# Kernel optimization log

Measured on AMD Instinct MI355X. Metric: run time of the kernel, lower is better.

Reference implementation:

```python
import jax, jax.numpy as jnp
import numpy as np

N_HEAD = 4
D_K = 64
D_V = 64
D_MODEL = 256
LN_EPS = 1e-5


def setup_inputs() -> dict:
    key = jax.random.key(0)
    k1, k2, k3 = jax.random.split(key, 3)
    B, C, H, W = 2, D_MODEL, 64, 64
    q = jax.random.normal(k1, (B, C, H, W), dtype=jnp.float32)
    # w_qkvs: Linear(d_model, n_head*d_k, bias=False), weight [out, in]
    std_qkv = np.sqrt(2.0 / (D_MODEL + D_K))
    w_qkv = jax.random.normal(k2, (N_HEAD * D_K, D_MODEL), dtype=jnp.float32) * std_qkv
    # fc: Linear(n_head*d_v, d_model), xavier-normal-ish init
    std_fc = np.sqrt(2.0 / (N_HEAD * D_V + D_MODEL))
    fc_w = jax.random.normal(k3, (D_MODEL, N_HEAD * D_V), dtype=jnp.float32) * std_fc
    fc_b = jnp.zeros((D_MODEL,), dtype=jnp.float32)
    ln_g = jnp.ones((D_MODEL,), dtype=jnp.float32)
    ln_b = jnp.zeros((D_MODEL,), dtype=jnp.float32)
    return {"q": q, "w_qkv": w_qkv, "fc_w": fc_w, "fc_b": fc_b, "ln_g": ln_g, "ln_b": ln_b}


def reference(q, w_qkv, fc_w, fc_b, ln_g, ln_b):
    B, C, H, W = q.shape
    L = H * W
    # [B, C, H, W] -> [B, L, C]
    x = q.reshape(B, C, L).transpose(0, 2, 1)
    residual = x
    # shared QKV projection (self-attention branch: q == k == v)
    qkv = x @ w_qkv.T                                  # [B, L, nh*dk]
    qh = qkv.reshape(B, L, N_HEAD, D_K).transpose(2, 0, 1, 3)  # [h, B, L, dk]
    scale = jnp.asarray(np.sqrt(D_K), dtype=q.dtype)
    attn = jnp.einsum('hbqd,hbkd->hbqk', qh, qh) / scale       # [h, B, L, L]
    attn = jax.nn.softmax(attn, axis=-1)
    out = jnp.einsum('hbqk,hbkd->hbqd', attn, qh)              # [h, B, L, dv]
    # [h, B, L, dv] -> [B, L, h*dv]
    out = out.transpose(1, 2, 0, 3).reshape(B, L, N_HEAD * D_V)
    out = out @ fc_w.T + fc_b
    out = out + residual
    mu = jnp.mean(out, axis=-1, keepdims=True)
    var = jnp.mean(jnp.square(out - mu), axis=-1, keepdims=True)
    out = (out - mu) / jnp.sqrt(var + LN_EPS) * ln_g + ln_b
    # raw row-major view back to [B, C, H, W] (matches torch .view)
    return out.reshape(B, -1, H, W)
```

## Files before the change

kernel.cpp:

```cpp
#include <hip/hip_runtime.h>

#define L_SEQ 4096
#define DMODEL 256
#define DH 64
#define NKB 16

typedef __attribute__((ext_vector_type(8))) __bf16 bf16x8;
typedef __attribute__((ext_vector_type(4))) float f32x4;
typedef __attribute__((ext_vector_type(16))) float f32x16;
typedef __attribute__((ext_vector_type(8))) unsigned short ushort8v;
typedef __attribute__((ext_vector_type(4))) unsigned short ushort4v;
typedef __attribute__((ext_vector_type(2))) unsigned int uint2v;
typedef __attribute__((ext_vector_type(4))) unsigned int uint4v;

__device__ __forceinline__ unsigned short f2bf(float f) {
  unsigned u = __builtin_bit_cast(unsigned, f);
  u += 0x7fffu + ((u >> 16) & 1u);
  return (unsigned short)(u >> 16);
}
__device__ __forceinline__ float bf2f(unsigned short h) {
  unsigned u = ((unsigned)h) << 16;
  return __builtin_bit_cast(float, u);
}
__device__ __forceinline__ bf16x8 ld_frag(const unsigned short* p) {
  return __builtin_bit_cast(bf16x8, *(const ushort8v*)p);
}
__device__ __forceinline__ unsigned cvtpk(float lo, float hi) {
  unsigned r;
  asm("v_cvt_pk_bf16_f32 %0, %1, %2" : "=v"(r) : "v"(lo), "v"(hi));
  return r;
}
__device__ __forceinline__ void plswap(unsigned& a, unsigned& b) {
  asm("v_permlane32_swap_b32 %0, %1" : "+v"(a), "+v"(b));
}
__device__ __forceinline__ float exp2raw(float x) {
  float r;
  asm("v_exp_f32 %0, %1" : "=v"(r) : "v"(x));
  return r;
}

__global__ __launch_bounds__(256) void k_transpose(const float* __restrict__ q,
                                                   unsigned short* __restrict__ xbf,
                                                   const float* __restrict__ w,
                                                   const float* __restrict__ fcw,
                                                   unsigned short* __restrict__ wbf,
                                                   unsigned short* __restrict__ fcwbf) {
  int bx = blockIdx.x;
  int t = threadIdx.x;
  if (bx >= 512) {
    int i = ((bx - 512) * 256 + t) * 4;
    float4 a = *(const float4*)(w + i);
    float4 b = *(const float4*)(fcw + i);
    ushort4v av = {f2bf(a.x), f2bf(a.y), f2bf(a.z), f2bf(a.w)};
    ushort4v bv = {f2bf(b.x), f2bf(b.y), f2bf(b.z), f2bf(b.w)};
    *(ushort4v*)(wbf + i) = av;
    *(ushort4v*)(fcwbf + i) = bv;
    return;
  }
  __shared__ float T[64 * 65];
  int b = bx >> 8, rest = bx & 255;
  int ct = rest >> 6, lt = rest & 63;
#pragma unroll
  for (int it = 0; it < 4; ++it) {
    int i = (t >> 4) + it * 16;
    int j0 = (t & 15) * 4;
    float4 v = *(const float4*)(q + ((size_t)(b * 256 + ct * 64 + i)) * 4096 + lt * 64 + j0);
    T[i * 65 + j0 + 0] = v.x;
    T[i * 65 + j0 + 1] = v.y;
    T[i * 65 + j0 + 2] = v.z;
    T[i * 65 + j0 + 3] = v.w;
  }
  __syncthreads();
#pragma unroll
  for (int it = 0; it < 2; ++it) {
    int l = (t >> 3) + it * 32;
    int c0 = (t & 7) * 8;
    ushort8v o;
#pragma unroll
    for (int k = 0; k < 8; ++k) o[k] = f2bf(T[(c0 + k) * 65 + l]);
    *(ushort8v*)(xbf + ((size_t)(b * 4096 + lt * 64 + l)) * 256 + ct * 64 + c0) = o;
  }
}

#define KP2 136
__global__ __launch_bounds__(256) void k_qkv(const unsigned short* __restrict__ xbf,
                                             const unsigned short* __restrict__ wbf,
                                             unsigned short* __restrict__ Qh,
                                             unsigned short* __restrict__ QhT) {
  __shared__ unsigned short As[64 * KP2];
  __shared__ unsigned short Bs[64 * KP2];
  int bx = blockIdx.x;
  int mtile = bx >> 2, h = bx & 3;
  int m0 = mtile * 64;
  int b = m0 >> 12, l0 = m0 & 4095;
  int t = threadIdx.x;
  int wv = t >> 6, lane = t & 63, g = lane >> 4, ln = lane & 15;
  f32x4 acc[4] = {};
  for (int kb = 0; kb < 2; ++kb) {
#pragma unroll
    for (int it = 0; it < 4; ++it) {
      int idx = t + it * 256;
      int row = idx >> 4;
      int c0 = (idx & 15) * 8;
      *(ushort8v*)(As + row * KP2 + c0) =
          *(const ushort8v*)(xbf + (size_t)(m0 + row) * 256 + kb * 128 + c0);
      *(ushort8v*)(Bs + row * KP2 + c0) =
          *(const ushort8v*)(wbf + (size_t)(h * 64 + row) * 256 + kb * 128 + c0);
    }
    __syncthreads();
#pragma unroll
    for (int kc = 0; kc < 4; ++kc) {
      bf16x8 a = ld_frag(As + (wv * 16 + ln) * KP2 + kc * 32 + g * 8);
#pragma unroll
      for (int tn = 0; tn < 4; ++tn) {
        bf16x8 bb = ld_frag(Bs + (tn * 16 + ln) * KP2 + kc * 32 + g * 8);
        acc[tn] = __builtin_amdgcn_mfma_f32_16x16x32_bf16(a, bb, acc[tn], 0, 0, 0);
      }
    }
    __syncthreads();
  }
  size_t pbase = (size_t)(b * 4 + h);
#pragma unroll
  for (int tn = 0; tn < 4; ++tn) {
#pragma unroll
    for (int r = 0; r < 4; ++r) {
      int lrow = wv * 16 + g * 4 + r;
      int d = tn * 16 + ln;
      unsigned short bv = f2bf(acc[tn][r]);
      As[lrow * 64 + (((d >> 3) ^ (lrow & 7)) * 8) + (d & 7)] = bv;
      Bs[d * 64 + (((lrow >> 3) ^ (d & 7)) * 8) + (lrow & 7)] = bv;
    }
  }
#pragma unroll
  for (int s = 0; s < 2; ++s) {
    int flat = s * 64 + lane;
    int lrow = wv * 16 + (flat >> 3);
    int c8 = lane & 7;
    ushort8v v = *(const ushort8v*)(As + lrow * 64 + ((c8 ^ (lrow & 7)) * 8));
    *(ushort8v*)(Qh + (pbase * L_SEQ + l0 + lrow) * DH + c8 * 8) = v;
  }
  __syncthreads();
#pragma unroll
  for (int s = 0; s < 2; ++s) {
    int flat = s * 256 + t;
    int drow = flat >> 3;
    int c8 = t & 7;
    ushort8v v = *(const ushort8v*)(Bs + drow * 64 + ((c8 ^ (drow & 7)) * 8));
    *(ushort8v*)(QhT + (pbase * DH + drow) * L_SEQ + l0 + c8 * 8) = v;
  }
}

__global__ __launch_bounds__(256, 2) void k_attn(const unsigned short* __restrict__ Qh,
                                                 const unsigned short* __restrict__ QhT,
                                                 unsigned short* __restrict__ Opart,
                                                 float* __restrict__ Lpart) {
  constexpr float C1 = 0.18033688011112042f;
  constexpr float C2 = -23.083120654223414f;
  __shared__ unsigned short smem[4 * 4096];
  int bx = blockIdx.x;
  int p = bx & 7;
  int u = bx >> 3;
  int qsup = u & 31, ks = u >> 5;
  int t = threadIdx.x;
  int wv = t >> 6, lane = t & 63, ln = lane & 31, hi = lane >> 5;
  const unsigned short* Qp = Qh + (size_t)p * L_SEQ * DH;
  const unsigned short* QTp = QhT + (size_t)p * DH * L_SEQ;
  int q0 = qsup * 128;
  int qw = q0 + wv * 32;

  bf16x8 aQ[4];
#pragma unroll
  for (int kq = 0; kq < 4; ++kq)
    aQ[kq] = ld_frag(Qp + (size_t)(qw + ln) * DH + kq * 16 + hi * 8);

  f32x16 oacc[2] = {};
  float lacc = 0.f;

  int srow0 = t >> 3, scol = t & 7;
  int srow1 = srow0 + 32;
  int sdst0 = srow0 * 64 + ((scol ^ (srow0 & 7)) * 8);
  int sdst1 = srow1 * 64 + ((scol ^ (srow1 & 7)) * 8);

  ushort8v kreg0, kreg1, vreg0, vreg1;
  {
    int kbase = (ks * NKB) * 64;
    kreg0 = *(const ushort8v*)(Qp + (size_t)(kbase + srow0) * DH + scol * 8);
    kreg1 = *(const ushort8v*)(Qp + (size_t)(kbase + srow1) * DH + scol * 8);
    vreg0 = *(const ushort8v*)(QTp + (size_t)srow0 * L_SEQ + kbase + scol * 8);
    vreg1 = *(const ushort8v*)(QTp + (size_t)srow1 * L_SEQ + kbase + scol * 8);
  }

  for (int kb = 0; kb < NKB; ++kb) {
    unsigned short* Kc = smem + (kb & 1) * 8192;
    unsigned short* Vc = Kc + 4096;
    *(ushort8v*)(Kc + sdst0) = kreg0;
    *(ushort8v*)(Kc + sdst1) = kreg1;
    *(ushort8v*)(Vc + sdst0) = vreg0;
    *(ushort8v*)(Vc + sdst1) = vreg1;
    __syncthreads();
    if (kb + 1 < NKB) {
      int kbase = (ks * NKB + kb + 1) * 64;
      kreg0 = *(const ushort8v*)(Qp + (size_t)(kbase + srow0) * DH + scol * 8);
      kreg1 = *(const ushort8v*)(Qp + (size_t)(kbase + srow1) * DH + scol * 8);
      vreg0 = *(const ushort8v*)(QTp + (size_t)srow0 * L_SEQ + kbase + scol * 8);
      vreg1 = *(const ushort8v*)(QTp + (size_t)srow1 * L_SEQ + kbase + scol * 8);
    }
#pragma unroll
    for (int mt = 0; mt < 2; ++mt) {
      int key = mt * 32 + ln;
      bf16x8 aK[4];
#pragma unroll
      for (int kq = 0; kq < 4; ++kq)
        aK[kq] = ld_frag(Kc + key * 64 + (((kq * 2 + hi) ^ (key & 7)) * 8));
      f32x16 s = {};
#pragma unroll
      for (int kq = 0; kq < 4; ++kq)
        s = __builtin_amdgcn_mfma_f32_32x32x16_bf16(aK[kq], aQ[kq], s, 0, 0, 0);
      float pv[16];
#pragma unroll
      for (int r = 0; r < 16; ++r) pv[r] = exp2raw(fmaf(s[r], C1, C2));
      lacc += (((pv[0] + pv[1]) + (pv[2] + pv[3])) + ((pv[4] + pv[5]) + (pv[6] + pv[7]))) +
              (((pv[8] + pv[9]) + (pv[10] + pv[11])) + ((pv[12] + pv[13]) + (pv[14] + pv[15])));
      unsigned w0 = cvtpk(pv[0], pv[1]), w1 = cvtpk(pv[2], pv[3]);
      unsigned w2 = cvtpk(pv[4], pv[5]), w3 = cvtpk(pv[6], pv[7]);
      unsigned w4 = cvtpk(pv[8], pv[9]), w5 = cvtpk(pv[10], pv[11]);
      unsigned w6 = cvtpk(pv[12], pv[13]), w7 = cvtpk(pv[14], pv[15]);
      plswap(w0, w2);
      plswap(w1, w3);
      plswap(w4, w6);
      plswap(w5, w7);
      uint4v c0 = {w0, w1, w2, w3};
      uint4v c1 = {w4, w5, w6, w7};
      bf16x8 pf0 = __builtin_bit_cast(bf16x8, c0);
      bf16x8 pf1 = __builtin_bit_cast(bf16x8, c1);
#pragma unroll
      for (int dt = 0; dt < 2; ++dt) {
        int d = dt * 32 + ln;
        bf16x8 vf0 = ld_frag(Vc + d * 64 + (((mt * 4 + 0 * 2 + hi) ^ (d & 7)) * 8));
        bf16x8 vf1 = ld_frag(Vc + d * 64 + (((mt * 4 + 1 * 2 + hi) ^ (d & 7)) * 8));
        oacc[dt] = __builtin_amdgcn_mfma_f32_32x32x16_bf16(vf0, pf0, oacc[dt], 0, 0, 0);
        oacc[dt] = __builtin_amdgcn_mfma_f32_32x32x16_bf16(vf1, pf1, oacc[dt], 0, 0, 0);
      }
    }
  }
  lacc += __shfl_xor(lacc, 32, 64);
  size_t pq = (size_t)(ks * 8 + p) * L_SEQ;
  if (lane < 32) Lpart[pq + qw + ln] = lacc;
#pragma unroll
  for (int dt = 0; dt < 2; ++dt) {
    size_t rb = (pq + qw + ln) * DH + dt * 32 + hi * 4;
#pragma unroll
    for (int g8 = 0; g8 < 4; ++g8) {
      uint2v wv2 = {cvtpk(oacc[dt][g8 * 4 + 0], oacc[dt][g8 * 4 + 1]),
                    cvtpk(oacc[dt][g8 * 4 + 2], oacc[dt][g8 * 4 + 3])};
      *(uint2v*)(Opart + rb + g8 * 8) = wv2;
    }
  }
}

#define CP 72
__global__ __launch_bounds__(256) void k_fc(const unsigned short* __restrict__ Opart,
                                            const float* __restrict__ Lpart,
                                            const unsigned short* __restrict__ fcwbf,
                                            const float* __restrict__ qres,
                                            const float* __restrict__ fcb,
                                            const float* __restrict__ lng,
                                            const float* __restrict__ lnb,
                                            float* __restrict__ out) {
  __shared__ unsigned short As[16 * CP];
  __shared__ unsigned short Bs[256 * CP];
  __shared__ float resT[256 * 17];
  __shared__ float outB[16 * 260];
  __shared__ float redS[4][16], redQ[4][16], muA[16], rsA[16];
  int bx = blockIdx.x;
  int m0 = bx * 16;
  int b = m0 >> 12, lpart = m0 & 4095;
  int t = threadIdx.x;
  int wv = t >> 6, lane = t & 63, g = lane >> 4, ln = lane & 15;

#pragma unroll
  for (int it = 0; it < 4; ++it) {
    int c = (t >> 2) + it * 64;
    int l4 = (t & 3) * 4;
    float4 v = *(const float4*)(qres + ((size_t)(b * 256 + c)) * 4096 + lpart + l4);
    resT[c * 17 + l4 + 0] = v.x;
    resT[c * 17 + l4 + 1] = v.y;
    resT[c * 17 + l4 + 2] = v.z;
    resT[c * 17 + l4 + 3] = v.w;
  }

  f32x4 acc[4] = {};
  for (int kb = 0; kb < 4; ++kb) {
    if (t < 128) {
      int row = t >> 3, c0 = (t & 7) * 8;
      int q = lpart + row;
      int p = b * 4 + kb;
      float lsum = Lpart[(size_t)(0 * 8 + p) * L_SEQ + q] +
                   Lpart[(size_t)(1 * 8 + p) * L_SEQ + q] +
                   Lpart[(size_t)(2 * 8 + p) * L_SEQ + q] +
                   Lpart[(size_t)(3 * 8 + p) * L_SEQ + q];
      float inv = 1.0f / lsum;
      float a8[8] = {0.f, 0.f, 0.f, 0.f, 0.f, 0.f, 0.f, 0.f};
#pragma unroll
      for (int ksp = 0; ksp < 4; ++ksp) {
        ushort8v v = *(const ushort8v*)(Opart + ((size_t)(ksp * 8 + p) * L_SEQ + q) * DH + c0);
#pragma unroll
        for (int j = 0; j < 8; ++j) a8[j] += bf2f(v[j]);
      }
      ushort8v o;
#pragma unroll
      for (int j = 0; j < 8; ++j) o[j] = f2bf(a8[j] * inv);
      *(ushort8v*)(As + row * CP + c0) = o;
    }
#pragma unroll
    for (int it = 0; it < 8; ++it) {
      int idx = t + it * 256;
      int row = idx >> 3, c0 = (idx & 7) * 8;
      *(ushort8v*)(Bs + row * CP + c0) =
          *(const ushort8v*)(fcwbf + (size_t)row * 256 + kb * 64 + c0);
    }
    __syncthreads();
#pragma unroll
    for (int kc = 0; kc < 2; ++kc) {
      bf16x8 a = ld_frag(As + ln * CP + kc * 32 + g * 8);
      bf16x8 bb[4];
#pragma unroll
      for (int tn = 0; tn < 4; ++tn) bb[tn] = ld_frag(Bs + (wv * 64 + tn * 16 + ln) * CP + kc * 32 + g * 8);
#pragma unroll
      for (int tn = 0; tn < 4; ++tn)
        acc[tn] = __builtin_amdgcn_mfma_f32_16x16x32_bf16(a, bb[tn], acc[tn], 0, 0, 0);
    }
    __syncthreads();
  }
  float fb[4], lg[4], lb[4];
#pragma unroll
  for (int tn = 0; tn < 4; ++tn) {
    int o = wv * 64 + tn * 16 + ln;
    fb[tn] = fcb[o]; lg[tn] = lng[o]; lb[tn] = lnb[o];
  }
  {
    float ps[4] = {0.f, 0.f, 0.f, 0.f}, pq2[4] = {0.f, 0.f, 0.f, 0.f};
#pragma unroll
    for (int tn = 0; tn < 4; ++tn) {
      int o = wv * 64 + tn * 16 + ln;
#pragma unroll
      for (int r = 0; r < 4; ++r) {
        float v = acc[tn][r] + fb[tn] + resT[o * 17 + g * 4 + r];
        acc[tn][r] = v;
        ps[r] += v;
        pq2[r] += v * v;
      }
    }
#pragma unroll
    for (int r = 0; r < 4; ++r) {
      float s = ps[r], q2 = pq2[r];
#pragma unroll
      for (int off = 1; off < 16; off <<= 1) {
        s += __shfl_xor(s, off, 64);
        q2 += __shfl_xor(q2, off, 64);
      }
      if (ln == 0) {
        int row = g * 4 + r;
        redS[wv][row] = s;
        redQ[wv][row] = q2;
      }
    }
  }
  __syncthreads();
  if (t < 16) {
    float s = redS[0][t] + redS[1][t] + redS[2][t] + redS[3][t];
    float q2 = redQ[0][t] + redQ[1][t] + redQ[2][t] + redQ[3][t];
    float mu = s * (1.f / 256.f);
    float var = q2 * (1.f / 256.f) - mu * mu;
    muA[t] = mu;
    rsA[t] = rsqrtf(var + 1e-5f);
  }
  __syncthreads();
#pragma unroll
  for (int r = 0; r < 4; ++r) {
    int row = g * 4 + r;
    float mu = muA[row], rs = rsA[row];
#pragma unroll
    for (int tn = 0; tn < 4; ++tn) {
      int o = wv * 64 + tn * 16 + ln;
      outB[row * 260 + o] = (acc[tn][r] - mu) * rs * lg[tn] + lb[tn];
    }
  }
  __syncthreads();
#pragma unroll
  for (int it = 0; it < 4; ++it) {
    int idx = it * 256 + t;
    int row = idx >> 6;
    int c4 = (idx & 63) * 4;
    float4 v = *(const float4*)(outB + row * 260 + c4);
    *(float4*)(out + (size_t)(m0 + row) * 256 + c4) = v;
  }
}

extern "C" void kernel_launch(void* const* d_in, const int* in_sizes, int n_in,
                              void* d_out, int out_size, void* d_ws, size_t ws_size,
                              hipStream_t stream) {
  const float* q = (const float*)d_in[0];
  const float* w_qkv = (const float*)d_in[1];
  const float* fc_w = (const float*)d_in[2];
  const float* fc_b = (const float*)d_in[3];
  const float* ln_g = (const float*)d_in[4];
  const float* ln_b = (const float*)d_in[5];
  float* out = (float*)d_out;

  unsigned short* wbf = (unsigned short*)d_ws;
  unsigned short* fcwbf = wbf + 65536;
  unsigned short* xbf = fcwbf + 65536;
  unsigned short* Qh = xbf + 2097152;
  unsigned short* QhT = Qh + 2097152;
  unsigned short* Opart = QhT + 2097152;
  float* Lpart = (float*)(Opart + 8388608);

  k_transpose<<<dim3(576), dim3(256), 0, stream>>>(q, xbf, w_qkv, fc_w, wbf, fcwbf);
  k_qkv<<<dim3(512), dim3(256), 0, stream>>>(xbf, wbf, Qh, QhT);
  k_attn<<<dim3(1024), dim3(256), 0, stream>>>(Qh, QhT, Opart, Lpart);
  k_fc<<<dim3(512), dim3(256), 0, stream>>>(Opart, Lpart, fcwbf, q, fc_b, ln_g, ln_b, out);
}
```

Baseline: 134.4 us.

## Fuse input transpose into QKV kernel and split attention keys across warps

Removes the separate transpose/convert kernel. k_qkv now reads the fp32 NCHW input and fp32 weights directly and converts them to bf16 while loading shared memory, and k_fc converts fc weights on the fly. The attention kernel moves to 512 threads, with two warp groups each handling half of every 64-key block, followed by a shared-memory reduction of the partial outputs and row sums. This cuts a launch and an intermediate round trip through global memory. In exchange it adds strided scalar shared-memory stores in the transpose, redundant weight conversion in every block, and an extra merge step in attention.

Measured after the change: 142.2 us. 1.06x slower.

```diff
diff --git a/kernel.cpp b/kernel.cpp
--- a/kernel.cpp
+++ b/kernel.cpp
@@ -39,52 +39,9 @@
   return r;
 }
 
-__global__ __launch_bounds__(256) void k_transpose(const float* __restrict__ q,
-                                                   unsigned short* __restrict__ xbf,
-                                                   const float* __restrict__ w,
-                                                   const float* __restrict__ fcw,
-                                                   unsigned short* __restrict__ wbf,
-                                                   unsigned short* __restrict__ fcwbf) {
-  int bx = blockIdx.x;
-  int t = threadIdx.x;
-  if (bx >= 512) {
-    int i = ((bx - 512) * 256 + t) * 4;
-    float4 a = *(const float4*)(w + i);
-    float4 b = *(const float4*)(fcw + i);
-    ushort4v av = {f2bf(a.x), f2bf(a.y), f2bf(a.z), f2bf(a.w)};
-    ushort4v bv = {f2bf(b.x), f2bf(b.y), f2bf(b.z), f2bf(b.w)};
-    *(ushort4v*)(wbf + i) = av;
-    *(ushort4v*)(fcwbf + i) = bv;
-    return;
-  }
-  __shared__ float T[64 * 65];
-  int b = bx >> 8, rest = bx & 255;
-  int ct = rest >> 6, lt = rest & 63;
-#pragma unroll
-  for (int it = 0; it < 4; ++it) {
-    int i = (t >> 4) + it * 16;
-    int j0 = (t & 15) * 4;
-    float4 v = *(const float4*)(q + ((size_t)(b * 256 + ct * 64 + i)) * 4096 + lt * 64 + j0);
-    T[i * 65 + j0 + 0] = v.x;
-    T[i * 65 + j0 + 1] = v.y;
-    T[i * 65 + j0 + 2] = v.z;
-    T[i * 65 + j0 + 3] = v.w;
-  }
-  __syncthreads();
-#pragma unroll
-  for (int it = 0; it < 2; ++it) {
-    int l = (t >> 3) + it * 32;
-    int c0 = (t & 7) * 8;
-    ushort8v o;
-#pragma unroll
-    for (int k = 0; k < 8; ++k) o[k] = f2bf(T[(c0 + k) * 65 + l]);
-    *(ushort8v*)(xbf + ((size_t)(b * 4096 + lt * 64 + l)) * 256 + ct * 64 + c0) = o;
-  }
-}
-
 #define KP2 136
-__global__ __launch_bounds__(256) void k_qkv(const unsigned short* __restrict__ xbf,
-                                             const unsigned short* __restrict__ wbf,
+__global__ __launch_bounds__(256) void k_qkv(const float* __restrict__ q,
+                                             const float* __restrict__ w,
                                              unsigned short* __restrict__ Qh,
                                              unsigned short* __restrict__ QhT) {
   __shared__ unsigned short As[64 * KP2];
@@ -95,17 +52,31 @@
   int b = m0 >> 12, l0 = m0 & 4095;
   int t = threadIdx.x;
   int wv = t >> 6, lane = t & 63, g = lane >> 4, ln = lane & 15;
+  int cA = t & 127, lh = t >> 7;
   f32x4 acc[4] = {};
   for (int kb = 0; kb < 2; ++kb) {
+    {
+      const float* qp = q + ((size_t)(b * 256 + kb * 128 + cA)) * 4096 + l0 + lh * 32;
+#pragma unroll
+      for (int j4 = 0; j4 < 8; ++j4) {
+        float4 v = *(const float4*)(qp + j4 * 4);
+        int lrow = lh * 32 + j4 * 4;
+        As[(lrow + 0) * KP2 + cA] = f2bf(v.x);
+        As[(lrow + 1) * KP2 + cA] = f2bf(v.y);
+        As[(lrow + 2) * KP2 + cA] = f2bf(v.z);
+        As[(lrow + 3) * KP2 + cA] = f2bf(v.w);
+      }
+    }
 #pragma unroll
     for (int it = 0; it < 4; ++it) {
       int idx = t + it * 256;
       int row = idx >> 4;
       int c0 = (idx & 15) * 8;
-      *(ushort8v*)(As + row * KP2 + c0) =
-          *(const ushort8v*)(xbf + (size_t)(m0 + row) * 256 + kb * 128 + c0);
-      *(ushort8v*)(Bs + row * KP2 + c0) =
-          *(const ushort8v*)(wbf + (size_t)(h * 64 + row) * 256 + kb * 128 + c0);
+      const float* wp = w + (size_t)(h * 64 + row) * 256 + kb * 128 + c0;
+      float4 wa = *(const float4*)(wp);
+      float4 wb = *(const float4*)(wp + 4);
+      uint4v pk = {cvtpk(wa.x, wa.y), cvtpk(wa.z, wa.w), cvtpk(wb.x, wb.y), cvtpk(wb.z, wb.w)};
+      *(uint4v*)(Bs + row * KP2 + c0) = pk;
     }
     __syncthreads();
 #pragma unroll
@@ -150,23 +121,25 @@
   }
 }
 
-__global__ __launch_bounds__(256, 2) void k_attn(const unsigned short* __restrict__ Qh,
+__global__ __launch_bounds__(512, 2) void k_attn(const unsigned short* __restrict__ Qh,
                                                  const unsigned short* __restrict__ QhT,
                                                  unsigned short* __restrict__ Opart,
                                                  float* __restrict__ Lpart) {
   constexpr float C1 = 0.18033688011112042f;
   constexpr float C2 = -23.083120654223414f;
   __shared__ unsigned short smem[4 * 4096];
+  __shared__ float lmerge[4][64];
   int bx = blockIdx.x;
   int p = bx & 7;
   int u = bx >> 3;
   int qsup = u & 31, ks = u >> 5;
   int t = threadIdx.x;
   int wv = t >> 6, lane = t & 63, ln = lane & 31, hi = lane >> 5;
+  int kw = wv >> 2, qh = wv & 3;
   const unsigned short* Qp = Qh + (size_t)p * L_SEQ * DH;
   const unsigned short* QTp = QhT + (size_t)p * DH * L_SEQ;
   int q0 = qsup * 128;
-  int qw = q0 + wv * 32;
+  int qw = q0 + qh * 32;
 
   bf16x8 aQ[4];
 #pragma unroll
@@ -176,84 +149,98 @@
   f32x16 oacc[2] = {};
   float lacc = 0.f;
 
-  int srow0 = t >> 3, scol = t & 7;
-  int srow1 = srow0 + 32;
-  int sdst0 = srow0 * 64 + ((scol ^ (srow0 & 7)) * 8);
-  int sdst1 = srow1 * 64 + ((scol ^ (srow1 & 7)) * 8);
-
-  ushort8v kreg0, kreg1, vreg0, vreg1;
+  int srow = t >> 3, scol = t & 7;
+  int sdst = srow * 64 + ((scol ^ (srow & 7)) * 8);
+
+  ushort8v kreg, vreg;
   {
     int kbase = (ks * NKB) * 64;
-    kreg0 = *(const ushort8v*)(Qp + (size_t)(kbase + srow0) * DH + scol * 8);
-    kreg1 = *(const ushort8v*)(Qp + (size_t)(kbase + srow1) * DH + scol * 8);
-    vreg0 = *(const ushort8v*)(QTp + (size_t)srow0 * L_SEQ + kbase + scol * 8);
-    vreg1 = *(const ushort8v*)(QTp + (size_t)srow1 * L_SEQ + kbase + scol * 8);
+    kreg = *(const ushort8v*)(Qp + (size_t)(kbase + srow) * DH + scol * 8);
+    vreg = *(const ushort8v*)(QTp + (size_t)srow * L_SEQ + kbase + scol * 8);
   }
 
   for (int kb = 0; kb < NKB; ++kb) {
     unsigned short* Kc = smem + (kb & 1) * 8192;
     unsigned short* Vc = Kc + 4096;
-    *(ushort8v*)(Kc + sdst0) = kreg0;
-    *(ushort8v*)(Kc + sdst1) = kreg1;
-    *(ushort8v*)(Vc + sdst0) = vreg0;
-    *(ushort8v*)(Vc + sdst1) = vreg1;
+    *(ushort8v*)(Kc + sdst) = kreg;
+    *(ushort8v*)(Vc + sdst) = vreg;
     __syncthreads();
     if (kb + 1 < NKB) {
       int kbase = (ks * NKB + kb + 1) * 64;
-      kreg0 = *(const ushort8v*)(Qp + (size_t)(kbase + srow0) * DH + scol * 8);
-      kreg1 = *(const ushort8v*)(Qp + (size_t)(kbase + srow1) * DH + scol * 8);
-      vreg0 = *(const ushort8v*)(QTp + (size_t)srow0 * L_SEQ + kbase + scol * 8);
-      vreg1 = *(const ushort8v*)(QTp + (size_t)srow1 * L_SEQ + kbase + scol * 8);
-    }
-#pragma unroll
-    for (int mt = 0; mt < 2; ++mt) {
-      int key = mt * 32 + ln;
-      bf16x8 aK[4];
-#pragma unroll
-      for (int kq = 0; kq < 4; ++kq)
-        aK[kq] = ld_frag(Kc + key * 64 + (((kq * 2 + hi) ^ (key & 7)) * 8));
-      f32x16 s = {};
-#pragma unroll
-      for (int kq = 0; kq < 4; ++kq)
-        s = __builtin_amdgcn_mfma_f32_32x32x16_bf16(aK[kq], aQ[kq], s, 0, 0, 0);
-      float pv[16];
-#pragma unroll
-      for (int r = 0; r < 16; ++r) pv[r] = exp2raw(fmaf(s[r], C1, C2));
-      lacc += (((pv[0] + pv[1]) + (pv[2] + pv[3])) + ((pv[4] + pv[5]) + (pv[6] + pv[7]))) +
-              (((pv[8] + pv[9]) + (pv[10] + pv[11])) + ((pv[12] + pv[13]) + (pv[14] + pv[15])));
-      unsigned w0 = cvtpk(pv[0], pv[1]), w1 = cvtpk(pv[2], pv[3]);
-      unsigned w2 = cvtpk(pv[4], pv[5]), w3 = cvtpk(pv[6], pv[7]);
-      unsigned w4 = cvtpk(pv[8], pv[9]), w5 = cvtpk(pv[10], pv[11]);
-      unsigned w6 = cvtpk(pv[12], pv[13]), w7 = cvtpk(pv[14], pv[15]);
-      plswap(w0, w2);
-      plswap(w1, w3);
-      plswap(w4, w6);
-      plswap(w5, w7);
-      uint4v c0 = {w0, w1, w2, w3};
-      uint4v c1 = {w4, w5, w6, w7};
-      bf16x8 pf0 = __builtin_bit_cast(bf16x8, c0);
-      bf16x8 pf1 = __builtin_bit_cast(bf16x8, c1);
-#pragma unroll
-      for (int dt = 0; dt < 2; ++dt) {
-        int d = dt * 32 + ln;
-        bf16x8 vf0 = ld_frag(Vc + d * 64 + (((mt * 4 + 0 * 2 + hi) ^ (d & 7)) * 8));
-        bf16x8 vf1 = ld_frag(Vc + d * 64 + (((mt * 4 + 1 * 2 + hi) ^ (d & 7)) * 8));
-        oacc[dt] = __builtin_amdgcn_mfma_f32_32x32x16_bf16(vf0, pf0, oacc[dt], 0, 0, 0);
-        oacc[dt] = __builtin_amdgcn_mfma_f32_32x32x16_bf16(vf1, pf1, oacc[dt], 0, 0, 0);
-      }
-    }
-  }
-  lacc += __shfl_xor(lacc, 32, 64);
-  size_t pq = (size_t)(ks * 8 + p) * L_SEQ;
-  if (lane < 32) Lpart[pq + qw + ln] = lacc;
-#pragma unroll
-  for (int dt = 0; dt < 2; ++dt) {
-    size_t rb = (pq + qw + ln) * DH + dt * 32 + hi * 4;
-#pragma unroll
-    for (int g8 = 0; g8 < 4; ++g8) {
-      uint2v wv2 = {cvtpk(oacc[dt][g8 * 4 + 0], oacc[dt][g8 * 4 + 1]),
-                    cvtpk(oacc[dt][g8 * 4 + 2], oacc[dt][g8 * 4 + 3])};
-      *(uint2v*)(Opart + rb + g8 * 8) = wv2;
+      kreg = *(const ushort8v*)(Qp + (size_t)(kbase + srow) * DH + scol * 8);
+      vreg = *(const ushort8v*)(QTp + (size_t)srow * L_SEQ + kbase + scol * 8);
+    }
+    int key = kw * 32 + ln;
+    bf16x8 aK[4];
+#pragma unroll
+    for (int kq = 0; kq < 4; ++kq)
+      aK[kq] = ld_frag(Kc + key * 64 + (((kq * 2 + hi) ^ (key & 7)) * 8));
+    f32x16 s = {};
+#pragma unroll
+    for (int kq = 0; kq < 4; ++kq)
+      s = __builtin_amdgcn_mfma_f32_32x32x16_bf16(aK[kq], aQ[kq], s, 0, 0, 0);
+    float pv[16];
+#pragma unroll
+    for (int r = 0; r < 16; ++r) pv[r] = exp2raw(fmaf(s[r], C1, C2));
+    lacc += (((pv[0] + pv[1]) + (pv[2] + pv[3])) + ((pv[4] + pv[5]) + (pv[6] + pv[7]))) +
+            (((pv[8] + pv[9]) + (pv[10] + pv[11])) + ((pv[12] + pv[13]) + (pv[14] + pv[15])));
+    unsigned w0 = cvtpk(pv[0], pv[1]), w1 = cvtpk(pv[2], pv[3]);
+    unsigned w2 = cvtpk(pv[4], pv[5]), w3 = cvtpk(pv[6], pv[7]);
+    unsigned w4 = cvtpk(pv[8], pv[9]), w5 = cvtpk(pv[10], pv[11]);
+    unsigned w6 = cvtpk(pv[12], pv[13]), w7 = cvtpk(pv[14], pv[15]);
+    plswap(w0, w2);
+    plswap(w1, w3);
+    plswap(w4, w6);
+    plswap(w5, w7);
+    uint4v c0 = {w0, w1, w2, w3};
+    uint4v c1 = {w4, w5, w6, w7};
+    bf16x8 pf0 = __builtin_bit_cast(bf16x8, c0);
+    bf16x8 pf1 = __builtin_bit_cast(bf16x8, c1);
+#pragma unroll
+    for (int dt = 0; dt < 2; ++dt) {
+      int d = dt * 32 + ln;
+      bf16x8 vf0 = ld_frag(Vc + d * 64 + (((kw * 4 + 0 + hi) ^ (d & 7)) * 8));
+      bf16x8 vf1 = ld_frag(Vc + d * 64 + (((kw * 4 + 2 + hi) ^ (d & 7)) * 8));
+      oacc[dt] = __builtin_amdgcn_mfma_f32_32x32x16_bf16(vf0, pf0, oacc[dt], 0, 0, 0);
+      oacc[dt] = __builtin_amdgcn_mfma_f32_32x32x16_bf16(vf1, pf1, oacc[dt], 0, 0, 0);
+    }
+  }
+  __syncthreads();
+  float* smf = (float*)smem;
+  if (kw == 1) {
+#pragma unroll
+    for (int dt = 0; dt < 2; ++dt)
+#pragma unroll
+      for (int g4 = 0; g4 < 4; ++g4) {
+        f32x4 c4 = {oacc[dt][g4 * 4 + 0], oacc[dt][g4 * 4 + 1],
+                    oacc[dt][g4 * 4 + 2], oacc[dt][g4 * 4 + 3]};
+        *(f32x4*)(smf + qh * 2048 + (dt * 4 + g4) * 256 + lane * 4) = c4;
+      }
+    lmerge[qh][lane] = lacc;
+  }
+  __syncthreads();
+  if (kw == 0) {
+#pragma unroll
+    for (int dt = 0; dt < 2; ++dt)
+#pragma unroll
+      for (int g4 = 0; g4 < 4; ++g4) {
+        f32x4 c4 = *(const f32x4*)(smf + qh * 2048 + (dt * 4 + g4) * 256 + lane * 4);
+#pragma unroll
+        for (int j = 0; j < 4; ++j) oacc[dt][g4 * 4 + j] += c4[j];
+      }
+    lacc += lmerge[qh][lane];
+    lacc += __shfl_xor(lacc, 32, 64);
+    size_t pq = (size_t)(ks * 8 + p) * L_SEQ;
+    if (lane < 32) Lpart[pq + qw + ln] = lacc;
+#pragma unroll
+    for (int dt = 0; dt < 2; ++dt) {
+      size_t rb = (pq + qw + ln) * DH + dt * 32 + hi * 4;
+#pragma unroll
+      for (int g8 = 0; g8 < 4; ++g8) {
+        uint2v wv2 = {cvtpk(oacc[dt][g8 * 4 + 0], oacc[dt][g8 * 4 + 1]),
+                      cvtpk(oacc[dt][g8 * 4 + 2], oacc[dt][g8 * 4 + 3])};
+        *(uint2v*)(Opart + rb + g8 * 8) = wv2;
+      }
     }
   }
 }
@@ -261,7 +248,7 @@
 #define CP 72
 __global__ __launch_bounds__(256) void k_fc(const unsigned short* __restrict__ Opart,
                                             const float* __restrict__ Lpart,
-                                            const unsigned short* __restrict__ fcwbf,
+                                            const float* __restrict__ fcw,
                                             const float* __restrict__ qres,
                                             const float* __restrict__ fcb,
                                             const float* __restrict__ lng,
@@ -316,8 +303,11 @@
     for (int it = 0; it < 8; ++it) {
       int idx = t + it * 256;
       int row = idx >> 3, c0 = (idx & 7) * 8;
-      *(ushort8v*)(Bs + row * CP + c0) =
-          *(const ushort8v*)(fcwbf + (size_t)row * 256 + kb * 64 + c0);
+      const float* wp = fcw + (size_t)row * 256 + kb * 64 + c0;
+      float4 wa = *(const float4*)(wp);
+      float4 wb = *(const float4*)(wp + 4);
+      uint4v pk = {cvtpk(wa.x, wa.y), cvtpk(wa.z, wa.w), cvtpk(wb.x, wb.y), cvtpk(wb.z, wb.w)};
+      *(uint4v*)(Bs + row * CP + c0) = pk;
     }
     __syncthreads();
 #pragma unroll
@@ -408,16 +398,12 @@
   const float* ln_b = (const float*)d_in[5];
   float* out = (float*)d_out;
 
-  unsigned short* wbf = (unsigned short*)d_ws;
-  unsigned short* fcwbf = wbf + 65536;
-  unsigned short* xbf = fcwbf + 65536;
-  unsigned short* Qh = xbf + 2097152;
+  unsigned short* Qh = (unsigned short*)d_ws;
   unsigned short* QhT = Qh + 2097152;
   unsigned short* Opart = QhT + 2097152;
   float* Lpart = (float*)(Opart + 8388608);
 
-  k_transpose<<<dim3(576), dim3(256), 0, stream>>>(q, xbf, w_qkv, fc_w, wbf, fcwbf);
-  k_qkv<<<dim3(512), dim3(256), 0, stream>>>(xbf, wbf, Qh, QhT);
-  k_attn<<<dim3(1024), dim3(256), 0, stream>>>(Qh, QhT, Opart, Lpart);
-  k_fc<<<dim3(512), dim3(256), 0, stream>>>(Opart, Lpart, fcwbf, q, fc_b, ln_g, ln_b, out);
-}
+  k_qkv<<<dim3(512), dim3(256), 0, stream>>>(q, w_qkv, Qh, QhT);
+  k_attn<<<dim3(1024), dim3(512), 0, stream>>>(Qh, QhT, Opart, Lpart);
+  k_fc<<<dim3(512), dim3(256), 0, stream>>>(Opart, Lpart, fc_w, q, fc_b, ln_g, ln_b, out);
+}
```

## Fuse input transpose and weight bf16 conversion into QKV and FC kernels

Applied to the files above, without the earlier changes.

Removes the separate transpose/convert kernel. The QKV kernel now reads fp32 input directly, transposes it through shared memory and converts to bf16. Both GEMM kernels convert fp32 weights to bf16 on the fly. This drops one launch and the xbf round-trip through global memory. In exchange, each of the 4 head blocks per m-tile re-reads and re-transposes the same input tile, weights are reconverted per block, and shared memory use rises, which may reduce occupancy.

Measured after the change: 137.0 us. Within noise of the previous version (+1.9%).

```diff
diff --git a/kernel.cpp b/kernel.cpp
--- a/kernel.cpp
+++ b/kernel.cpp
@@ -39,54 +39,12 @@
   return r;
 }
 
-__global__ __launch_bounds__(256) void k_transpose(const float* __restrict__ q,
-                                                   unsigned short* __restrict__ xbf,
-                                                   const float* __restrict__ w,
-                                                   const float* __restrict__ fcw,
-                                                   unsigned short* __restrict__ wbf,
-                                                   unsigned short* __restrict__ fcwbf) {
-  int bx = blockIdx.x;
-  int t = threadIdx.x;
-  if (bx >= 512) {
-    int i = ((bx - 512) * 256 + t) * 4;
-    float4 a = *(const float4*)(w + i);
-    float4 b = *(const float4*)(fcw + i);
-    ushort4v av = {f2bf(a.x), f2bf(a.y), f2bf(a.z), f2bf(a.w)};
-    ushort4v bv = {f2bf(b.x), f2bf(b.y), f2bf(b.z), f2bf(b.w)};
-    *(ushort4v*)(wbf + i) = av;
-    *(ushort4v*)(fcwbf + i) = bv;
-    return;
-  }
-  __shared__ float T[64 * 65];
-  int b = bx >> 8, rest = bx & 255;
-  int ct = rest >> 6, lt = rest & 63;
-#pragma unroll
-  for (int it = 0; it < 4; ++it) {
-    int i = (t >> 4) + it * 16;
-    int j0 = (t & 15) * 4;
-    float4 v = *(const float4*)(q + ((size_t)(b * 256 + ct * 64 + i)) * 4096 + lt * 64 + j0);
-    T[i * 65 + j0 + 0] = v.x;
-    T[i * 65 + j0 + 1] = v.y;
-    T[i * 65 + j0 + 2] = v.z;
-    T[i * 65 + j0 + 3] = v.w;
-  }
-  __syncthreads();
-#pragma unroll
-  for (int it = 0; it < 2; ++it) {
-    int l = (t >> 3) + it * 32;
-    int c0 = (t & 7) * 8;
-    ushort8v o;
-#pragma unroll
-    for (int k = 0; k < 8; ++k) o[k] = f2bf(T[(c0 + k) * 65 + l]);
-    *(ushort8v*)(xbf + ((size_t)(b * 4096 + lt * 64 + l)) * 256 + ct * 64 + c0) = o;
-  }
-}
-
 #define KP2 136
-__global__ __launch_bounds__(256) void k_qkv(const unsigned short* __restrict__ xbf,
-                                             const unsigned short* __restrict__ wbf,
+__global__ __launch_bounds__(256) void k_qkv(const float* __restrict__ q,
+                                             const float* __restrict__ w,
                                              unsigned short* __restrict__ Qh,
                                              unsigned short* __restrict__ QhT) {
+  __shared__ float T[128 * 65];
   __shared__ unsigned short As[64 * KP2];
   __shared__ unsigned short Bs[64 * KP2];
   int bx = blockIdx.x;
@@ -98,14 +56,36 @@
   f32x4 acc[4] = {};
   for (int kb = 0; kb < 2; ++kb) {
 #pragma unroll
+    for (int it = 0; it < 8; ++it) {
+      int i = (t >> 4) + it * 16;
+      int j0 = (t & 15) * 4;
+      float4 v = *(const float4*)(q + ((size_t)(b * 256 + kb * 128 + i)) * 4096 + l0 + j0);
+      T[i * 65 + j0 + 0] = v.x;
+      T[i * 65 + j0 + 1] = v.y;
+      T[i * 65 + j0 + 2] = v.z;
+      T[i * 65 + j0 + 3] = v.w;
+    }
+#pragma unroll
     for (int it = 0; it < 4; ++it) {
       int idx = t + it * 256;
       int row = idx >> 4;
       int c0 = (idx & 15) * 8;
-      *(ushort8v*)(As + row * KP2 + c0) =
-          *(const ushort8v*)(xbf + (size_t)(m0 + row) * 256 + kb * 128 + c0);
-      *(ushort8v*)(Bs + row * KP2 + c0) =
-          *(const ushort8v*)(wbf + (size_t)(h * 64 + row) * 256 + kb * 128 + c0);
+      const float* wp = w + (size_t)(h * 64 + row) * 256 + kb * 128 + c0;
+      float4 wa = *(const float4*)(wp);
+      float4 wb = *(const float4*)(wp + 4);
+      uint4v pk = {cvtpk(wa.x, wa.y), cvtpk(wa.z, wa.w), cvtpk(wb.x, wb.y), cvtpk(wb.z, wb.w)};
+      *(uint4v*)(Bs + row * KP2 + c0) = pk;
+    }
+    __syncthreads();
+#pragma unroll
+    for (int it = 0; it < 4; ++it) {
+      int idx = t + it * 256;
+      int row = idx >> 4;
+      int c0 = (idx & 15) * 8;
+      ushort8v o;
+#pragma unroll
+      for (int k = 0; k < 8; ++k) o[k] = f2bf(T[(c0 + k) * 65 + row]);
+      *(ushort8v*)(As + row * KP2 + c0) = o;
     }
     __syncthreads();
 #pragma unroll
@@ -261,7 +241,7 @@
 #define CP 72
 __global__ __launch_bounds__(256) void k_fc(const unsigned short* __restrict__ Opart,
                                             const float* __restrict__ Lpart,
-                                            const unsigned short* __restrict__ fcwbf,
+                                            const float* __restrict__ fcw,
                                             const float* __restrict__ qres,
                                             const float* __restrict__ fcb,
                                             const float* __restrict__ lng,
@@ -316,8 +296,11 @@
     for (int it = 0; it < 8; ++it) {
       int idx = t + it * 256;
       int row = idx >> 3, c0 = (idx & 7) * 8;
-      *(ushort8v*)(Bs + row * CP + c0) =
-          *(const ushort8v*)(fcwbf + (size_t)row * 256 + kb * 64 + c0);
+      const float* wp = fcw + (size_t)row * 256 + kb * 64 + c0;
+      float4 wa = *(const float4*)(wp);
+      float4 wb = *(const float4*)(wp + 4);
+      uint4v pk = {cvtpk(wa.x, wa.y), cvtpk(wa.z, wa.w), cvtpk(wb.x, wb.y), cvtpk(wb.z, wb.w)};
+      *(uint4v*)(Bs + row * CP + c0) = pk;
     }
     __syncthreads();
 #pragma unroll
@@ -408,16 +391,12 @@
   const float* ln_b = (const float*)d_in[5];
   float* out = (float*)d_out;
 
-  unsigned short* wbf = (unsigned short*)d_ws;
-  unsigned short* fcwbf = wbf + 65536;
-  unsigned short* xbf = fcwbf + 65536;
-  unsigned short* Qh = xbf + 2097152;
+  unsigned short* Qh = (unsigned short*)d_ws;
   unsigned short* QhT = Qh + 2097152;
   unsigned short* Opart = QhT + 2097152;
   float* Lpart = (float*)(Opart + 8388608);
 
-  k_transpose<<<dim3(576), dim3(256), 0, stream>>>(q, xbf, w_qkv, fc_w, wbf, fcwbf);
-  k_qkv<<<dim3(512), dim3(256), 0, stream>>>(xbf, wbf, Qh, QhT);
+  k_qkv<<<dim3(512), dim3(256), 0, stream>>>(q, w_qkv, Qh, QhT);
   k_attn<<<dim3(1024), dim3(256), 0, stream>>>(Qh, QhT, Opart, Lpart);
-  k_fc<<<dim3(512), dim3(256), 0, stream>>>(Opart, Lpart, fcwbf, q, fc_b, ln_g, ln_b, out);
-}
+  k_fc<<<dim3(512), dim3(256), 0, stream>>>(Opart, Lpart, fc_w, q, fc_b, ln_g, ln_b, out);
+}
```
